# Kernel optimization log

Hardware: AMD Instinct MI355X
Metric: run time of the kernel (lower is better)

Reference implementation:

```python
import math
import jax, jax.numpy as jnp
import numpy as np

NUM_BUCKETS = 32
MAX_DISTANCE = 128
N_HEADS = 16
D_KV = 64


def _relative_position_bucket(rel_pos, num_buckets=NUM_BUCKETS, max_distance=MAX_DISTANCE):
    # bidirectional=True branch of T5's bucketing
    num_buckets = num_buckets // 2
    rel_buckets = (rel_pos > 0).astype(jnp.int32) * num_buckets
    rel_pos = jnp.abs(rel_pos)
    max_exact = num_buckets // 2
    is_small = rel_pos < max_exact
    # safe log (values < max_exact are masked out by is_small)
    rp_f = jnp.maximum(rel_pos, 1).astype(jnp.float32)
    rel_if_large = max_exact + (
        jnp.log(rp_f / max_exact) / math.log(max_distance / max_exact) * (num_buckets - max_exact)
    ).astype(jnp.int32)
    rel_if_large = jnp.minimum(rel_if_large, num_buckets - 1)
    return rel_buckets + jnp.where(is_small, rel_pos, rel_if_large)


def compute_bias(rel_bias_table, q_len, k_len):
    ctx = jnp.arange(q_len)[:, None]
    mem = jnp.arange(k_len)[None, :]
    buckets = _relative_position_bucket(mem - ctx)  # [q, k]
    values = rel_bias_table[buckets]                # [q, k, h]
    return jnp.transpose(values, (2, 0, 1))[None]   # [1, h, q, k]


def setup_inputs() -> dict:
    key = jax.random.key(0)
    k1, k2, k3, k4 = jax.random.split(key, 4)
    d_model = 1024
    return {
        "hidden_states": jax.random.normal(k1, (2, 2048, d_model), jnp.float32),
        "w_qkv": jax.random.normal(k2, (d_model, 3 * N_HEADS * D_KV), jnp.float32) * (d_model ** -0.5),
        "w_o": jax.random.normal(k3, (N_HEADS * D_KV, d_model), jnp.float32) * ((N_HEADS * D_KV) ** -0.5),
        "rel_bias_table": jax.random.normal(k4, (NUM_BUCKETS, N_HEADS), jnp.float32),
    }


def reference(hidden_states, w_qkv, w_o, rel_bias_table):
    b, s, _ = hidden_states.shape
    inner = N_HEADS * D_KV
    qkv = hidden_states @ w_qkv                         # [b, s, 3*inner]
    q, k, v = jnp.split(qkv, [inner, 2 * inner], axis=-1)
    def to_bhsd(x):
        return jnp.transpose(x.reshape(b, s, N_HEADS, D_KV), (0, 2, 1, 3))
    q, k, v = to_bhsd(q), to_bhsd(k), to_bhsd(v)
    scores = jnp.einsum("bhqd,bhkd->bhqk", q, k)        # no 1/sqrt(d) scaling in T5
    position_bias = compute_bias(rel_bias_table, s, s)  # [1, h, q, k]
    scores = scores + position_bias
    attn = jax.nn.softmax(scores.astype(jnp.float32), axis=-1).astype(scores.dtype)
    out = jnp.einsum("bhqk,bhkd->bhqd", attn, v)
    out = jnp.transpose(out, (0, 2, 1, 3)).reshape(b, s, inner)
    attn_output = out @ w_o
    return attn_output, position_bias
```

## Files before the change

### kernel.cpp

```cpp
#include <hip/hip_runtime.h>
#include <hip/hip_bf16.h>
#include <cstdint>
#include <cstddef>

#define S_LEN 2048
#define NH 16
#define DKV 64
#define BATCH 2
#define DMODEL 1024

typedef _Float16 half_t;
typedef __attribute__((ext_vector_type(4))) _Float16 halfx4;
typedef __attribute__((ext_vector_type(8))) _Float16 half8;
typedef __attribute__((ext_vector_type(4))) float floatx4;

__device__ __forceinline__ void load_lds16(const half_t* g, half_t* l) {
  __builtin_amdgcn_global_load_lds((const __attribute__((address_space(1))) void*)g,
                                   (__attribute__((address_space(3))) void*)l, 16, 0, 0);
}

__device__ __forceinline__ int t5_bucket(int delta) {
  int base = (delta > 0) ? 16 : 0;
  int a = delta < 0 ? -delta : delta;
  int n;
  if (a < 8)       n = a;
  else if (a < 12) n = 8;
  else if (a < 16) n = 9;
  else if (a < 23) n = 10;
  else if (a < 32) n = 11;
  else if (a < 46) n = 12;
  else if (a < 64) n = 13;
  else if (a < 91) n = 14;
  else             n = 15;
  return base + n;
}

__global__ __launch_bounds__(256) void bias_kernel(const float* __restrict__ table,
                                                   float* __restrict__ out) {
  int h = blockIdx.x >> 11;
  int q = blockIdx.x & (S_LEN - 1);
  __shared__ float tb[32];
  if (threadIdx.x < 32) tb[threadIdx.x] = table[threadIdx.x * NH + h];
  __syncthreads();
  float* dst = out + (size_t)blockIdx.x * S_LEN;
  int k0 = threadIdx.x * 4;
#pragma unroll
  for (int half = 0; half < 2; half++) {
    int k = k0 + half * 1024;
    float4 v;
    v.x = tb[t5_bucket((k + 0) - q)];
    v.y = tb[t5_bucket((k + 1) - q)];
    v.z = tb[t5_bucket((k + 2) - q)];
    v.w = tb[t5_bucket((k + 3) - q)];
    *(float4*)(dst + k) = v;
  }
}

__global__ __launch_bounds__(256) void cast_f2h(const float* __restrict__ in,
                                                half_t* __restrict__ out) {
  int i = blockIdx.x * 256 + threadIdx.x;
  float4 v = ((const float4*)in)[i];
  halfx4 h;
  h[0] = (half_t)v.x; h[1] = (half_t)v.y; h[2] = (half_t)v.z; h[3] = (half_t)v.w;
  ((halfx4*)out)[i] = h;
}

__global__ __launch_bounds__(256) void transpose_cast(const float* __restrict__ in,
                                                      half_t* __restrict__ out,
                                                      int R, int C) {
  __shared__ float t[32][33];
  int lr = threadIdx.x >> 3;
  int lc = (threadIdx.x & 7) * 4;
  int r0 = blockIdx.y * 32, c0 = blockIdx.x * 32;
  float4 v = *(const float4*)(in + (size_t)(r0 + lr) * C + c0 + lc);
  t[lr][lc + 0] = v.x; t[lr][lc + 1] = v.y; t[lr][lc + 2] = v.z; t[lr][lc + 3] = v.w;
  __syncthreads();
  halfx4 hv;
#pragma unroll
  for (int u = 0; u < 4; u++) hv[u] = (half_t)t[lc + u][lr];
  *(halfx4*)(out + (size_t)(c0 + lr) * R + r0 + lc) = hv;
}

__global__ __launch_bounds__(256) void vtrans(const half_t* __restrict__ V,
                                              half_t* __restrict__ Vt) {
  __shared__ half_t T[64 * 72];
  const int bh = blockIdx.y;
  const int s0 = blockIdx.x * 64;
  const half_t* src = V + ((size_t)bh * S_LEN + s0) * DKV;
  half_t* dst = Vt + (size_t)bh * DKV * S_LEN + s0;
  const int sr = threadIdx.x >> 3;
  const int dc = (threadIdx.x & 7) * 8;
#pragma unroll
  for (int p = 0; p < 2; p++) {
    int s = sr + p * 32;
    half8 v = *(const half8*)(src + (size_t)s * DKV + dc);
#pragma unroll
    for (int u = 0; u < 8; u++) T[(dc + u) * 72 + s] = v[u];
  }
  __syncthreads();
#pragma unroll
  for (int p = 0; p < 2; p++) {
    int d = sr + p * 32;
    half8 v = *(half8*)&T[d * 72 + dc];
    *(half8*)(dst + (size_t)d * S_LEN + dc) = v;
  }
}

template <int MODE>
__global__ __launch_bounds__(256) void hgemm128(const half_t* __restrict__ A,
                                                const half_t* __restrict__ Bt,
                                                float* __restrict__ C,
                                                half_t* __restrict__ Qo,
                                                half_t* __restrict__ Ko,
                                                half_t* __restrict__ Vo,
                                                int M, int N, int K) {
  __shared__ half_t Asl[8 * 512];
  __shared__ half_t Bsl[8 * 512];

  const int tid = threadIdx.x;
  const int w = tid >> 6;
  const int lane = tid & 63;
  const int l15 = lane & 15;
  const int quad = lane >> 4;
  const int wm = w >> 1, wn = w & 1;
  const int m0 = blockIdx.y * 128;
  const int n0 = blockIdx.x * 128;

  floatx4 acc[4][4];
#pragma unroll
  for (int i = 0; i < 4; i++)
#pragma unroll
    for (int j = 0; j < 4; j++) acc[i][j] = (floatx4){0.f, 0.f, 0.f, 0.f};

  const half_t* ga0 = A + (size_t)(m0 + (2 * w + 0) * 16 + l15) * K + quad * 8;
  const half_t* ga1 = A + (size_t)(m0 + (2 * w + 1) * 16 + l15) * K + quad * 8;
  const half_t* gb0 = Bt + (size_t)(n0 + (2 * w + 0) * 16 + l15) * K + quad * 8;
  const half_t* gb1 = Bt + (size_t)(n0 + (2 * w + 1) * 16 + l15) * K + quad * 8;
  half_t* la0 = &Asl[(2 * w + 0) * 512];
  half_t* la1 = &Asl[(2 * w + 1) * 512];
  half_t* lb0 = &Bsl[(2 * w + 0) * 512];
  half_t* lb1 = &Bsl[(2 * w + 1) * 512];

  for (int k0 = 0; k0 < K; k0 += 32) {
    __syncthreads();
    load_lds16(ga0 + k0, la0);
    load_lds16(ga1 + k0, la1);
    load_lds16(gb0 + k0, lb0);
    load_lds16(gb1 + k0, lb1);
    __syncthreads();

    half8 af[4], bf[4];
#pragma unroll
    for (int i = 0; i < 4; i++) af[i] = *(half8*)&Asl[(wm * 4 + i) * 512 + lane * 8];
#pragma unroll
    for (int j = 0; j < 4; j++) bf[j] = *(half8*)&Bsl[(wn * 4 + j) * 512 + lane * 8];
#pragma unroll
    for (int i = 0; i < 4; i++)
#pragma unroll
      for (int j = 0; j < 4; j++)
        acc[i][j] = __builtin_amdgcn_mfma_f32_16x16x32_f16(af[i], bf[j], acc[i][j], 0, 0, 0);
  }

  const int rowbase = m0 + wm * 64;
  const int colbase = n0 + wn * 64;
  if (MODE == 0) {
#pragma unroll
    for (int i = 0; i < 4; i++)
#pragma unroll
      for (int j = 0; j < 4; j++)
#pragma unroll
        for (int r = 0; r < 4; r++)
          C[(size_t)(rowbase + i * 16 + quad * 4 + r) * N + colbase + j * 16 + l15] =
              acc[i][j][r];
  } else {
    const int which = colbase >> 10;
    const int h = (colbase & 1023) >> 6;
    const int b = rowbase >> 11;
    const int s0 = rowbase & (S_LEN - 1);
    half_t* base = ((which == 0) ? Qo : (which == 1) ? Ko : Vo) +
                   (size_t)(b * NH + h) * S_LEN * DKV;
#pragma unroll
    for (int i = 0; i < 4; i++)
#pragma unroll
      for (int j = 0; j < 4; j++)
#pragma unroll
        for (int r = 0; r < 4; r++)
          base[(size_t)(s0 + i * 16 + quad * 4 + r) * DKV + j * 16 + l15] =
              (half_t)acc[i][j][r];
  }
}

__global__ __launch_bounds__(256) void attn_mfma(const half_t* __restrict__ Q,
                                                 const half_t* __restrict__ K,
                                                 const half_t* __restrict__ Vt,
                                                 const float* __restrict__ table,
                                                 half_t* __restrict__ X) {
  __shared__ half_t Ks[64 * 64];
  __shared__ half_t Vts[64 * 64];
  __shared__ half_t Ps[64 * 68];
  __shared__ float tb[32];
  __shared__ float ebias[184];

  const int tid = threadIdx.x;
  const int w = tid >> 6;
  const int lane = tid & 63;
  const int l15 = lane & 15;
  const int quad = lane >> 4;
  const int bh = blockIdx.y;
  const int h = bh & (NH - 1);
  const int b = bh >> 4;
  const int q0 = blockIdx.x * 64;

  if (tid < 32) tb[tid] = table[tid * NH + h];
  __syncthreads();
  if (tid < 183) ebias[tid] = __expf(tb[t5_bucket(tid - 91)]);

  half8 qf[2];
#pragma unroll
  for (int ks = 0; ks < 2; ks++)
    qf[ks] = *(const half8*)(Q + ((size_t)bh * S_LEN + q0 + w * 16 + l15) * DKV +
                             ks * 32 + quad * 8);

  floatx4 o[4];
  float m[4], l[4];
#pragma unroll
  for (int r = 0; r < 4; r++) { m[r] = -1e30f; l[r] = 0.0f; }
#pragma unroll
  for (int nb = 0; nb < 4; nb++) o[nb] = (floatx4){0.f, 0.f, 0.f, 0.f};

  const int jr = tid >> 2;
  const int ub = (tid & 3) * 2;

  for (int kc = 0; kc < S_LEN; kc += 64) {
    __syncthreads();
    {
      const half_t* Kg = K + ((size_t)bh * S_LEN + kc + jr) * DKV + ub * 8;
      const half_t* Vg = Vt + ((size_t)bh * DKV + jr) * S_LEN + kc + ub * 8;
      half8 k0v = *(const half8*)(Kg);
      half8 k1v = *(const half8*)(Kg + 8);
      half8 v0v = *(const half8*)(Vg);
      half8 v1v = *(const half8*)(Vg + 8);
      int sw = jr & 7;
      *(half8*)&Ks[jr * 64 + ((ub + 0) ^ sw) * 8] = k0v;
      *(half8*)&Ks[jr * 64 + ((ub + 1) ^ sw) * 8] = k1v;
      *(half8*)&Vts[jr * 64 + ((ub + 0) ^ sw) * 8] = v0v;
      *(half8*)&Vts[jr * 64 + ((ub + 1) ^ sw) * 8] = v1v;
    }
    __syncthreads();

    floatx4 s[4];
#pragma unroll
    for (int nb = 0; nb < 4; nb++) {
      s[nb] = (floatx4){0.f, 0.f, 0.f, 0.f};
      int key = nb * 16 + l15;
      int sw = key & 7;
#pragma unroll
      for (int ks = 0; ks < 2; ks++) {
        half8 bf = *(half8*)&Ks[key * 64 + ((ks * 4 + quad) ^ sw) * 8];
        s[nb] = __builtin_amdgcn_mfma_f32_16x16x32_f16(qf[ks], bf, s[nb], 0, 0, 0);
      }
    }

    float al[4];
#pragma unroll
    for (int r = 0; r < 4; r++) {
      int qabs = q0 + w * 16 + quad * 4 + r;
      int db = kc + l15 - qabs + 91;
      float cm = fmaxf(fmaxf(s[0][r], s[1][r]), fmaxf(s[2][r], s[3][r]));
#pragma unroll
      for (int msk = 1; msk <= 8; msk <<= 1) cm = fmaxf(cm, __shfl_xor(cm, msk));
      float mn = fmaxf(m[r], cm);
      al[r] = __expf(m[r] - mn);
      m[r] = mn;
      float psum = 0.0f;
#pragma unroll
      for (int nb = 0; nb < 4; nb++) {
        int idx = db + nb * 16;
        idx = idx < 0 ? 0 : (idx > 182 ? 182 : idx);
        float p = __expf(s[nb][r] - mn) * ebias[idx];
        psum += p;
        Ps[(w * 16 + quad * 4 + r) * 68 + nb * 16 + l15] = (half_t)p;
      }
#pragma unroll
      for (int msk = 1; msk <= 8; msk <<= 1) psum += __shfl_xor(psum, msk);
      l[r] = l[r] * al[r] + psum;
#pragma unroll
      for (int nb = 0; nb < 4; nb++) o[nb][r] *= al[r];
    }

    half8 af[2];
#pragma unroll
    for (int ks = 0; ks < 2; ks++)
      af[ks] = *(half8*)&Ps[(w * 16 + l15) * 68 + ks * 32 + quad * 8];
#pragma unroll
    for (int nb = 0; nb < 4; nb++) {
      int dd = nb * 16 + l15;
      int sw = dd & 7;
#pragma unroll
      for (int ks = 0; ks < 2; ks++) {
        half8 bf = *(half8*)&Vts[dd * 64 + ((ks * 4 + quad) ^ sw) * 8];
        o[nb] = __builtin_amdgcn_mfma_f32_16x16x32_f16(af[ks], bf, o[nb], 0, 0, 0);
      }
    }
  }

#pragma unroll
  for (int r = 0; r < 4; r++) {
    int q = q0 + w * 16 + quad * 4 + r;
    float inv = 1.0f / l[r];
    half_t* dst = X + (size_t)(b * S_LEN + q) * DMODEL + h * DKV;
#pragma unroll
    for (int nb = 0; nb < 4; nb++) dst[nb * 16 + l15] = (half_t)(o[nb][r] * inv);
  }
}

extern "C" void kernel_launch(void* const* d_in, const int* in_sizes, int n_in,
                              void* d_out, int out_size, void* d_ws, size_t ws_size,
                              hipStream_t stream) {
  const float* hidden = (const float*)d_in[0];
  const float* w_qkv = (const float*)d_in[1];
  const float* w_o = (const float*)d_in[2];
  const float* table = (const float*)d_in[3];

  float* attn_out = (float*)d_out;
  float* bias_out = (float*)d_out + 4194304;

  half_t* Ah  = (half_t*)d_ws;
  half_t* Wqt = Ah + 4194304;
  half_t* Wot = Wqt + 3145728;
  half_t* Qh  = Wot + 1048576;
  half_t* Kh  = Qh + 4194304;
  half_t* Vh  = Kh + 4194304;
  half_t* Xh  = Vh + 4194304;
  half_t* Vth = Ah;

  cast_f2h<<<4096, 256, 0, stream>>>(hidden, Ah);
  transpose_cast<<<dim3(3072 / 32, 1024 / 32), 256, 0, stream>>>(w_qkv, Wqt, 1024, 3072);
  transpose_cast<<<dim3(1024 / 32, 1024 / 32), 256, 0, stream>>>(w_o, Wot, 1024, 1024);
  bias_kernel<<<NH * S_LEN, 256, 0, stream>>>(table, bias_out);

  hgemm128<1><<<dim3(3072 / 128, 4096 / 128), 256, 0, stream>>>(
      Ah, Wqt, nullptr, Qh, Kh, Vh, 4096, 3072, 1024);

  vtrans<<<dim3(S_LEN / 64, BATCH * NH), 256, 0, stream>>>(Vh, Vth);

  attn_mfma<<<dim3(S_LEN / 64, BATCH * NH), 256, 0, stream>>>(Qh, Kh, Vth, table, Xh);

  hgemm128<0><<<dim3(1024 / 128, 4096 / 128), 256, 0, stream>>>(
      Xh, Wot, attn_out, nullptr, nullptr, nullptr, 4096, 1024, 1024);
}
```

Baseline: 538.1 us.

## Split attention over key halves with a combine pass and fast-path constant bias

The attention kernel now splits each query tile's key range into two halves and runs them as separate blocks. This doubles the grid from 1024 to 2048 blocks to improve occupancy across CUs. Each block writes fp32 partial outputs plus its row max and sum, and a new combine kernel merges them with log-sum-exp rescaling into the fp16 X buffer. It also adds a fast path for key tiles far from the diagonal, where the bias is constant, skipping the per-element bucket index lookup. The cost is an extra launch and about 32 MB of fp32 partial traffic to write and read back.

New measurement: 525.3 us. 1.02x faster.

```diff
diff --git a/kernel.cpp b/kernel.cpp
--- a/kernel.cpp
+++ b/kernel.cpp
@@ -190,11 +190,13 @@
   }
 }
 
-__global__ __launch_bounds__(256) void attn_mfma(const half_t* __restrict__ Q,
-                                                 const half_t* __restrict__ K,
-                                                 const half_t* __restrict__ Vt,
-                                                 const float* __restrict__ table,
-                                                 half_t* __restrict__ X) {
+__global__ __launch_bounds__(256) void attn_split(const half_t* __restrict__ Q,
+                                                  const half_t* __restrict__ K,
+                                                  const half_t* __restrict__ Vt,
+                                                  const float* __restrict__ table,
+                                                  float* __restrict__ Opart,
+                                                  float* __restrict__ Mp,
+                                                  float* __restrict__ Lp) {
   __shared__ half_t Ks[64 * 64];
   __shared__ half_t Vts[64 * 64];
   __shared__ half_t Ps[64 * 68];
@@ -208,8 +210,9 @@
   const int quad = lane >> 4;
   const int bh = blockIdx.y;
   const int h = bh & (NH - 1);
-  const int b = bh >> 4;
-  const int q0 = blockIdx.x * 64;
+  const int part = blockIdx.x & 1;
+  const int q0 = (blockIdx.x >> 1) * 64;
+  const int q0w = q0 + w * 16;
 
   if (tid < 32) tb[tid] = table[tid * NH + h];
   __syncthreads();
@@ -218,7 +221,7 @@
   half8 qf[2];
 #pragma unroll
   for (int ks = 0; ks < 2; ks++)
-    qf[ks] = *(const half8*)(Q + ((size_t)bh * S_LEN + q0 + w * 16 + l15) * DKV +
+    qf[ks] = *(const half8*)(Q + ((size_t)bh * S_LEN + q0w + l15) * DKV +
                              ks * 32 + quad * 8);
 
   floatx4 o[4];
@@ -230,8 +233,9 @@
 
   const int jr = tid >> 2;
   const int ub = (tid & 3) * 2;
-
-  for (int kc = 0; kc < S_LEN; kc += 64) {
+  const int kbase = part * 1024;
+
+  for (int kc = kbase; kc < kbase + 1024; kc += 64) {
     __syncthreads();
     {
       const half_t* Kg = K + ((size_t)bh * S_LEN + kc + jr) * DKV + ub * 8;
@@ -261,31 +265,57 @@
       }
     }
 
+    const int rel = kc - q0w;
     float al[4];
-#pragma unroll
-    for (int r = 0; r < 4; r++) {
-      int qabs = q0 + w * 16 + quad * 4 + r;
-      int db = kc + l15 - qabs + 91;
-      float cm = fmaxf(fmaxf(s[0][r], s[1][r]), fmaxf(s[2][r], s[3][r]));
-#pragma unroll
-      for (int msk = 1; msk <= 8; msk <<= 1) cm = fmaxf(cm, __shfl_xor(cm, msk));
-      float mn = fmaxf(m[r], cm);
-      al[r] = __expf(m[r] - mn);
-      m[r] = mn;
-      float psum = 0.0f;
-#pragma unroll
-      for (int nb = 0; nb < 4; nb++) {
-        int idx = db + nb * 16;
-        idx = idx < 0 ? 0 : (idx > 182 ? 182 : idx);
-        float p = __expf(s[nb][r] - mn) * ebias[idx];
-        psum += p;
-        Ps[(w * 16 + quad * 4 + r) * 68 + nb * 16 + l15] = (half_t)p;
+    if (rel >= 106 || rel <= -154) {
+      const float eb = ebias[rel >= 106 ? 182 : 0];
+#pragma unroll
+      for (int r = 0; r < 4; r++) {
+        float cm = fmaxf(fmaxf(s[0][r], s[1][r]), fmaxf(s[2][r], s[3][r]));
+#pragma unroll
+        for (int msk = 1; msk <= 8; msk <<= 1) cm = fmaxf(cm, __shfl_xor(cm, msk));
+        float mn = fmaxf(m[r], cm);
+        al[r] = __expf(m[r] - mn);
+        m[r] = mn;
+        float psum = 0.0f;
+#pragma unroll
+        for (int nb = 0; nb < 4; nb++) {
+          float p = __expf(s[nb][r] - mn) * eb;
+          psum += p;
+          Ps[(w * 16 + quad * 4 + r) * 68 + nb * 16 + l15] = (half_t)p;
+        }
+#pragma unroll
+        for (int msk = 1; msk <= 8; msk <<= 1) psum += __shfl_xor(psum, msk);
+        l[r] = l[r] * al[r] + psum;
+#pragma unroll
+        for (int nb = 0; nb < 4; nb++) o[nb][r] *= al[r];
       }
-#pragma unroll
-      for (int msk = 1; msk <= 8; msk <<= 1) psum += __shfl_xor(psum, msk);
-      l[r] = l[r] * al[r] + psum;
-#pragma unroll
-      for (int nb = 0; nb < 4; nb++) o[nb][r] *= al[r];
+    } else {
+#pragma unroll
+      for (int r = 0; r < 4; r++) {
+        int qabs = q0w + quad * 4 + r;
+        int db = kc + l15 - qabs + 91;
+        float cm = fmaxf(fmaxf(s[0][r], s[1][r]), fmaxf(s[2][r], s[3][r]));
+#pragma unroll
+        for (int msk = 1; msk <= 8; msk <<= 1) cm = fmaxf(cm, __shfl_xor(cm, msk));
+        float mn = fmaxf(m[r], cm);
+        al[r] = __expf(m[r] - mn);
+        m[r] = mn;
+        float psum = 0.0f;
+#pragma unroll
+        for (int nb = 0; nb < 4; nb++) {
+          int idx = db + nb * 16;
+          idx = idx < 0 ? 0 : (idx > 182 ? 182 : idx);
+          float p = __expf(s[nb][r] - mn) * ebias[idx];
+          psum += p;
+          Ps[(w * 16 + quad * 4 + r) * 68 + nb * 16 + l15] = (half_t)p;
+        }
+#pragma unroll
+        for (int msk = 1; msk <= 8; msk <<= 1) psum += __shfl_xor(psum, msk);
+        l[r] = l[r] * al[r] + psum;
+#pragma unroll
+        for (int nb = 0; nb < 4; nb++) o[nb][r] *= al[r];
+      }
     }
 
     half8 af[2];
@@ -306,12 +336,34 @@
 
 #pragma unroll
   for (int r = 0; r < 4; r++) {
-    int q = q0 + w * 16 + quad * 4 + r;
-    float inv = 1.0f / l[r];
-    half_t* dst = X + (size_t)(b * S_LEN + q) * DMODEL + h * DKV;
-#pragma unroll
-    for (int nb = 0; nb < 4; nb++) dst[nb * 16 + l15] = (half_t)(o[nb][r] * inv);
-  }
+    int row = bh * S_LEN + q0w + quad * 4 + r;
+    float* op = Opart + (size_t)part * 4194304 + (size_t)row * 64;
+#pragma unroll
+    for (int nb = 0; nb < 4; nb++) op[nb * 16 + l15] = o[nb][r];
+    if (l15 == 0) {
+      Mp[part * 65536 + row] = m[r];
+      Lp[part * 65536 + row] = l[r];
+    }
+  }
+}
+
+__global__ __launch_bounds__(256) void attn_combine(const float* __restrict__ Opart,
+                                                    const float* __restrict__ Mp,
+                                                    const float* __restrict__ Lp,
+                                                    half_t* __restrict__ X) {
+  int idx = blockIdx.x * 256 + threadIdx.x;
+  int row = idx >> 6;
+  int d = idx & 63;
+  float m0 = Mp[row], m1 = Mp[65536 + row];
+  float l0 = Lp[row], l1 = Lp[65536 + row];
+  float M = fmaxf(m0, m1);
+  float a0 = __expf(m0 - M), a1 = __expf(m1 - M);
+  float L = l0 * a0 + l1 * a1;
+  float o = (Opart[(size_t)row * 64 + d] * a0 +
+             Opart[4194304 + (size_t)row * 64 + d] * a1) / L;
+  int bh = row >> 11, q = row & (S_LEN - 1);
+  int b = bh >> 4, h = bh & (NH - 1);
+  X[(size_t)(b * S_LEN + q) * DMODEL + h * DKV + d] = (half_t)o;
 }
 
 extern "C" void kernel_launch(void* const* d_in, const int* in_sizes, int n_in,
@@ -333,6 +385,9 @@
   half_t* Vh  = Kh + 4194304;
   half_t* Xh  = Vh + 4194304;
   half_t* Vth = Ah;
+  float* Opart = (float*)(Xh + 4194304);
+  float* Mpp   = Opart + 8388608;
+  float* Lpp   = Mpp + 131072;
 
   cast_f2h<<<4096, 256, 0, stream>>>(hidden, Ah);
   transpose_cast<<<dim3(3072 / 32, 1024 / 32), 256, 0, stream>>>(w_qkv, Wqt, 1024, 3072);
@@ -344,7 +399,9 @@
 
   vtrans<<<dim3(S_LEN / 64, BATCH * NH), 256, 0, stream>>>(Vh, Vth);
 
-  attn_mfma<<<dim3(S_LEN / 64, BATCH * NH), 256, 0, stream>>>(Qh, Kh, Vth, table, Xh);
+  attn_split<<<dim3((S_LEN / 64) * 2, BATCH * NH), 256, 0, stream>>>(
+      Qh, Kh, Vth, table, Opart, Mpp, Lpp);
+  attn_combine<<<4194304 / 256, 256, 0, stream>>>(Opart, Mpp, Lpp, Xh);
 
   hgemm128<0><<<dim3(1024 / 128, 4096 / 128), 256, 0, stream>>>(
       Xh, Wot, attn_out, nullptr, nullptr, nullptr, 4096, 1024, 1024);
```
